# Kernel optimization log

Hardware: AMD Instinct MI355X
Metric: run time of the kernel (lower is better)

## Reference

```python
import jax, jax.numpy as jnp
import numpy as np

BN_EPS = 1e-5


def fps(xyz, npoint):
    # farthest point sampling; xyz: (B,N,3) -> (B,npoint) int32, starts at index 0 (torch convention)
    B, N, _ = xyz.shape
    def step(carry, _):
        dist, last = carry
        lp = jnp.take_along_axis(xyz, last[:, None, None], axis=1)  # (B,1,3)
        d = jnp.sum((xyz - lp) ** 2, -1)                             # (B,N)
        dist = jnp.minimum(dist, d)
        nxt = jnp.argmax(dist, -1).astype(jnp.int32)
        return (dist, nxt), nxt
    init = (jnp.full((B, N), 1e10, xyz.dtype), jnp.zeros((B,), jnp.int32))
    _, rest = jax.lax.scan(step, init, None, length=npoint - 1)
    return jnp.concatenate([jnp.zeros((1, B), jnp.int32), rest], 0).T  # (B,npoint)


def knn_idx(xyz, centers, k):
    # xyz (B,N,3), centers (B,S,3) -> (B,S,k) nearest-neighbor indices
    d = (jnp.sum(centers ** 2, -1)[:, :, None]
         + jnp.sum(xyz ** 2, -1)[:, None, :]
         - 2.0 * jnp.einsum('bsc,bnc->bsn', centers, xyz))
    _, idx = jax.lax.top_k(-d, k)
    return idx


def group(feat, idx):
    # feat (B,N,C), idx (B,S,K) -> (B,S,K,C)
    return jax.vmap(lambda f, i: f[i])(feat, idx)


def sa_knn(xyz, points, npoint, nsample, w1, b1, w2, b2):
    # xyz (B,N,3), points (B,N,C); returns new_xyz (B,S,3), new_points (B,S,Cout)
    fidx = fps(xyz, npoint)
    new_xyz = jnp.take_along_axis(xyz, fidx[:, :, None], axis=1)        # (B,S,3)
    idx = knn_idx(xyz, new_xyz, nsample)                                 # (B,S,K)
    g_xyz = group(xyz, idx) - new_xyz[:, :, None, :]                     # relative coords
    g_pts = group(points, idx)
    x = jnp.concatenate([g_xyz, g_pts], -1)                              # (B,S,K,3+C)
    x = jax.nn.relu(jnp.einsum('bskc,oc->bsko', x, w1) + b1)
    x = jnp.einsum('bskc,oc->bsko', x, w2) + b2                          # last conv: no activation
    return new_xyz, jnp.max(x, 2)                                        # max over neighbors


def sa_all(xyz, points, w1, b1, w2, b2):
    # group_all: concat xyz+points over all N, shared MLP, max over N -> (B,Cout)
    x = jnp.concatenate([xyz, points], -1)                               # (B,N,3+C)
    x = jax.nn.relu(jnp.einsum('bnc,oc->bno', x, w1) + b1)
    x = jnp.einsum('bnc,oc->bno', x, w2) + b2
    return jnp.max(x, 1)


def fc_head(x, w1, b1, g1, be1, w2, b2, g2, be2):
    # Linear + BN(eval, running mean=0/var=1) + ReLU, twice; Dropout = identity in eval
    s = 1.0 / np.sqrt(1.0 + BN_EPS)
    x = jax.nn.relu(g1 * ((x @ w1.T + b1) * s) + be1)
    x = jax.nn.relu(g2 * ((x @ w2.T + b2) * s) + be2)
    return x


def forward(point_cloud, sa1_w1, sa1_b1, sa1_w2, sa1_b2,
            sa2_w1, sa2_b1, sa2_w2, sa2_b2,
            sa3_w1, sa3_b1, sa3_w2, sa3_b2,
            fc_w1, fc_b1, fc_g1, fc_be1, fc_w2, fc_b2, fc_g2, fc_be2):
    xyz = jnp.transpose(point_cloud, (0, 2, 1))  # (B,N,3)
    nsamples2 = (16, 32, 48)
    logits, codes = [], []
    for i in range(3):  # three structurally distinct branches
        x1, p1 = sa_knn(xyz, xyz, 512, 16, sa1_w1[i], sa1_b1[i], sa1_w2[i], sa1_b2[i])
        x2, p2 = sa_knn(x1, p1, 128, nsamples2[i], sa2_w1[i], sa2_b1[i], sa2_w2[i], sa2_b2[i])
        code = sa_all(x2, p2, sa3_w1[i], sa3_b1[i], sa3_w2[i], sa3_b2[i])   # (B,512)
        logits.append(fc_head(code, fc_w1[i], fc_b1[i], fc_g1[i], fc_be1[i],
                              fc_w2[i], fc_b2[i], fc_g2[i], fc_be2[i]))      # (B,128)
        codes.append(code)
    return tuple(logits) + tuple(codes)


def setup_inputs():
    key = jax.random.key(0)
    ks = iter(jax.random.split(key, 16))
    def w(shape, s=0.05):
        return jax.random.normal(next(ks), shape, jnp.float32) * s
    B, N = 32, 2048
    inp = {'point_cloud': jax.random.normal(next(ks), (B, 3, N), jnp.float32)}
    inp.update(
        sa1_w1=w((3, 64, 6)), sa1_b1=jnp.zeros((3, 64)), sa1_w2=w((3, 128, 64)), sa1_b2=jnp.zeros((3, 128)),
        sa2_w1=w((3, 128, 131)), sa2_b1=jnp.zeros((3, 128)), sa2_w2=w((3, 256, 128)), sa2_b2=jnp.zeros((3, 256)),
        sa3_w1=w((3, 512, 259)), sa3_b1=jnp.zeros((3, 512)), sa3_w2=w((3, 512, 512)), sa3_b2=jnp.zeros((3, 512)),
        fc_w1=w((3, 256, 512)), fc_b1=jnp.zeros((3, 256)), fc_g1=jnp.ones((3, 256)), fc_be1=jnp.zeros((3, 256)),
        fc_w2=w((3, 128, 256)), fc_b2=jnp.zeros((3, 128)), fc_g2=jnp.ones((3, 128)), fc_be2=jnp.zeros((3, 128)),
    )
    return inp


def reference(point_cloud, sa1_w1, sa1_b1, sa1_w2, sa1_b2,
              sa2_w1, sa2_b1, sa2_w2, sa2_b2,
              sa3_w1, sa3_b1, sa3_w2, sa3_b2,
              fc_w1, fc_b1, fc_g1, fc_be1, fc_w2, fc_b2, fc_g2, fc_be2):
    return forward(point_cloud, sa1_w1, sa1_b1, sa1_w2, sa1_b2,
                   sa2_w1, sa2_b1, sa2_w2, sa2_b2,
                   sa3_w1, sa3_b1, sa3_w2, sa3_b2,
                   fc_w1, fc_b1, fc_g1, fc_be1, fc_w2, fc_b2, fc_g2, fc_be2)
```

## Files before the change

kernel.cpp:

```cpp
#include <hip/hip_runtime.h>
#include <hip/hip_bf16.h>
#include <math.h>

#define DEVI __device__ __forceinline__

static constexpr int BB = 32, NN = 2048, S1 = 512, S2 = 128;

typedef float f32x4 __attribute__((ext_vector_type(4)));
typedef short s16x8 __attribute__((ext_vector_type(8)));

static constexpr size_t OFF_XS   = 0;
static constexpr size_t OFF_YS   = OFF_XS + (size_t)BB*NN;
static constexpr size_t OFF_ZS   = OFF_YS + (size_t)BB*NN;
static constexpr size_t OFF_SSQ  = OFF_ZS + (size_t)BB*NN;
static constexpr size_t OFF_NX1X = OFF_SSQ + (size_t)BB*NN;
static constexpr size_t OFF_NX1Y = OFF_NX1X + (size_t)BB*S1;
static constexpr size_t OFF_NX1Z = OFF_NX1Y + (size_t)BB*S1;
static constexpr size_t OFF_NX2X = OFF_NX1Z + (size_t)BB*S1;
static constexpr size_t OFF_NX2Y = OFF_NX2X + (size_t)BB*S2;
static constexpr size_t OFF_NX2Z = OFF_NX2Y + (size_t)BB*S2;
static constexpr size_t OFF_CODE = OFF_NX2Z + (size_t)BB*S2;
static constexpr size_t OFF_O3P  = OFF_CODE + (size_t)3*BB*512;
static constexpr size_t OFF_P1   = OFF_O3P + (size_t)3*BB*4*512;
static constexpr size_t OFF_X3   = OFF_P1 + (size_t)3*BB*S1*128;
static constexpr size_t OFF_H3   = OFF_X3 + (size_t)3*BB*S2*260;
static constexpr size_t OFF_W    = OFF_H3 + (size_t)3*BB*S2*512;
static constexpr size_t W1A  = OFF_W;
static constexpr size_t B1A  = W1A + 3*64*6;
static constexpr size_t W2A  = B1A + 3*64;
static constexpr size_t B2A  = W2A + 3*128*64;
static constexpr size_t W1B  = B2A + 3*128;
static constexpr size_t B1B  = W1B + 3*128*132;
static constexpr size_t W2B  = B1B + 3*128;
static constexpr size_t B2B  = W2B + 3*256*128;
static constexpr size_t W1C  = B2B + 3*256;
static constexpr size_t B1C  = W1C + 3*512*260;
static constexpr size_t W2C  = B1C + 3*512;
static constexpr size_t B2C  = W2C + 3*512*512;
static constexpr size_t FW1  = B2C + 3*512;
static constexpr size_t FB1  = FW1 + 3*256*512;
static constexpr size_t FG1  = FB1 + 3*256;
static constexpr size_t FBE1 = FG1 + 3*256;
static constexpr size_t FW2  = FBE1 + 3*256;
static constexpr size_t FB2  = FW2 + 3*128*256;
static constexpr size_t FG2  = FB2 + 3*128;
static constexpr size_t FBE2 = FG2 + 3*128;
static constexpr size_t OFF_KNN1 = FBE2 + 3*128;
static constexpr size_t OFF_KNN2 = OFF_KNN1 + (size_t)BB*S1*16;
static constexpr size_t OFF_W1BF = OFF_KNN2 + (size_t)BB*S2*48;
static constexpr size_t OFF_W2BF = OFF_W1BF + 30720;
static constexpr size_t OFF_W1CBH = OFF_W2BF + 49152;
static constexpr size_t OFF_W1CBL = OFF_W1CBH + 221184;
static constexpr size_t OFF_W2CBH = OFF_W1CBL + 221184;
static constexpr size_t OFF_W2CBL = OFF_W2CBH + 393216;
static constexpr size_t OFF_X3BH  = OFF_W2CBL + 393216;
static constexpr size_t OFF_X3BL  = OFF_X3BH + 1769472;
static constexpr size_t OFF_H3BH  = OFF_X3BL + 1769472;
static constexpr size_t OFF_H3BL  = OFF_H3BH + 3145728;
static constexpr size_t OFF_W2ABH = OFF_H3BL + 3145728;
static constexpr size_t OFF_W2ABL = OFF_W2ABH + 12288;
static constexpr size_t WS_FLOATS = OFF_W2ABL + 12288;

__device__ __align__(16) float g_ws[WS_FLOATS];
__device__ int g_is_f32;
__device__ int g_flip;
__device__ int g_bad;
__device__ int g_nz;

DEVI float bf2f(const __hip_bfloat16 v){ return __bfloat162float(v); }
DEVI float rn_add(float a, float b){ return __fadd_rn(a,b); }
DEVI float rn_mul(float a, float b){ return __fmul_rn(a,b); }
DEVI float rn_sub(float a, float b){ return __fsub_rn(a,b); }
DEVI float sq3(float x,float y,float z){ return rn_add(rn_add(rn_mul(x,x),rn_mul(y,y)),rn_mul(z,z)); }

DEVI float ldany(const void* s, size_t i, int isf){
  return isf ? ((const float*)s)[i] : bf2f(((const __hip_bfloat16*)s)[i]);
}
DEVI unsigned short f2bf(float f){
  unsigned u = __float_as_uint(f);
  unsigned r = (u + 0x7FFFu + ((u>>16)&1u)) >> 16;
  return (unsigned short)r;
}
DEVI float bfbits2f(unsigned short h){ return __uint_as_float(((unsigned)h)<<16); }
DEVI void mfma16(f32x4& d, s16x8 a, s16x8 b){
  asm volatile("v_mfma_f32_16x16x32_bf16 %0, %1, %2, %0" : "+v"(d) : "v"(a), "v"(b));
}
DEVI void mfma_guard(f32x4& d){
  asm volatile("s_nop 7\n\ts_nop 7\n\ts_nop 2" : "+v"(d));
}

#define DPPF(dst, src, CTRL) dst = __uint_as_float((unsigned)__builtin_amdgcn_update_dpp(\
    (int)__float_as_uint(src), (int)__float_as_uint(src), CTRL, 0xF, 0xF, false))
#define DPPI(dst, src, CTRL) dst = __builtin_amdgcn_update_dpp(src, src, CTRL, 0xF, 0xF, false)
#define RED_STEP(CTRL) { float ov; int oi; DPPF(ov, best, CTRL); DPPI(oi, bidx, CTRL); \
  if (ov > best || (ov == best && oi < bidx)){ best = ov; bidx = oi; } }
#define WAVE_ARGMAX() RED_STEP(0xB1) RED_STEP(0x4E) RED_STEP(0x124) RED_STEP(0x128) RED_STEP(0x142) RED_STEP(0x143)

#define REDMIN_STEP(CTRL) { float ov; int oi; DPPF(ov, best, CTRL); DPPI(oi, bidx, CTRL); \
  if (ov < best || (ov == best && oi < bidx)){ best = ov; bidx = oi; } }
#define WAVE_ARGMIN() REDMIN_STEP(0xB1) REDMIN_STEP(0x4E) REDMIN_STEP(0x124) REDMIN_STEP(0x128) REDMIN_STEP(0x142) REDMIN_STEP(0x143)

__global__ __launch_bounds__(256) void init_detect_kernel(const void* __restrict__ pc){
  __shared__ int s_cnt[256];
  int t = threadIdx.x;
  if (t==0){ g_flip=0; g_bad=0; g_nz=0; }
  const unsigned short* h = (const unsigned short*)pc;
  int weird = 0;
  for (int i=t; i<4096; i+=256){
    unsigned short v = h[2*i];
    int e = (v >> 7) & 0xFF;
    if (e == 0xFF || e < 90 || e > 140) weird++;
  }
  s_cnt[t] = weird; __syncthreads();
  for (int o=128;o>0;o>>=1){ if (t<o) s_cnt[t]+=s_cnt[t+o]; __syncthreads(); }
  if (t==0) g_is_f32 = (s_cnt[0] > 1024) ? 1 : 0;
}

struct ParamPtrs { const void* p[20]; };

DEVI void cvt_arr(const void* s, float* d, int n, int g, int gs, int isf){
  for (int i=g;i<n;i+=gs) d[i] = ldany(s,i,isf);
}
DEVI void cvt_pad(const void* s, float* d, int rows, int cin, int cinp, int g, int gs, int isf){
  int tot = rows*cinp;
  for (int i=g;i<tot;i+=gs){ int r=i/cinp, c=i%cinp; d[i] = (c<cin)? ldany(s,(size_t)r*cin+c,isf) : 0.f; }
}

__global__ __launch_bounds__(256) void cvtprep_kernel(ParamPtrs pp, const void* __restrict__ pc, int mode){
  if (mode==1 && g_flip==0) return;
  const int isf = g_is_f32 ^ mode;
  if (blockIdx.x < 256){
    int i = blockIdx.x*256 + threadIdx.x;
    int b = i >> 11, n = i & 2047;
    float x = ldany(pc, (size_t)(b*3+0)*2048 + n, isf);
    float y = ldany(pc, (size_t)(b*3+1)*2048 + n, isf);
    float z = ldany(pc, (size_t)(b*3+2)*2048 + n, isf);
    g_ws[OFF_XS+i]=x; g_ws[OFF_YS+i]=y; g_ws[OFF_ZS+i]=z;
    g_ws[OFF_SSQ+i]=sq3(x,y,z);
    return;
  }
  int g = (blockIdx.x-256)*256 + threadIdx.x; int gs = 512*256;
  float* ws = g_ws;
  cvt_arr(pp.p[0],  ws+W1A, 3*64*6, g, gs, isf);
  cvt_arr(pp.p[1],  ws+B1A, 3*64, g, gs, isf);
  cvt_arr(pp.p[2],  ws+W2A, 3*128*64, g, gs, isf);
  cvt_arr(pp.p[3],  ws+B2A, 3*128, g, gs, isf);
  cvt_pad(pp.p[4],  ws+W1B, 3*128, 131, 132, g, gs, isf);
  cvt_arr(pp.p[5],  ws+B1B, 3*128, g, gs, isf);
  cvt_arr(pp.p[6],  ws+W2B, 3*256*128, g, gs, isf);
  cvt_arr(pp.p[7],  ws+B2B, 3*256, g, gs, isf);
  cvt_pad(pp.p[8],  ws+W1C, 3*512, 259, 260, g, gs, isf);
  cvt_arr(pp.p[9],  ws+B1C, 3*512, g, gs, isf);
  cvt_arr(pp.p[10], ws+W2C, 3*512*512, g, gs, isf);
  cvt_arr(pp.p[11], ws+B2C, 3*512, g, gs, isf);
  cvt_arr(pp.p[12], ws+FW1, 3*256*512, g, gs, isf);
  cvt_arr(pp.p[13], ws+FB1, 3*256, g, gs, isf);
  cvt_arr(pp.p[14], ws+FG1, 3*256, g, gs, isf);
  cvt_arr(pp.p[15], ws+FBE1,3*256, g, gs, isf);
  cvt_arr(pp.p[16], ws+FW2, 3*128*256, g, gs, isf);
  cvt_arr(pp.p[17], ws+FB2, 3*128, g, gs, isf);
  cvt_arr(pp.p[18], ws+FG2, 3*128, g, gs, isf);
  cvt_arr(pp.p[19], ws+FBE2,3*128, g, gs, isf);
}

__global__ __launch_bounds__(256) void scan_check_kernel(){
  size_t off; int n, g, gs;
  if (blockIdx.x < 128){ off = OFF_XS; n = 3*BB*NN; g = blockIdx.x*256 + threadIdx.x; gs = 128*256; }
  else { off = FW1; n = 3*256*512; g = (blockIdx.x-128)*256 + threadIdx.x; gs = 128*256; }
  int bad=0, nz=0;
  for (int i=g;i<n;i+=gs){
    float v = g_ws[off + i];
    if (v != v || fabsf(v) > 1e4f) bad=1;
    if (fabsf(v) > 1e-20f) nz=1;
  }
  unsigned long long mb = __ballot(bad), mn = __ballot(nz);
  if ((threadIdx.x & 63)==0){
    if (mb) atomicOr(&g_bad, 1);
    if (mn) atomicOr(&g_nz, 1);
  }
}

__global__ __launch_bounds__(64) void resolve_flip_kernel(){
  if (threadIdx.x==0){
    g_flip = (g_bad || !g_nz) ? 1 : 0;
    g_bad = 0; g_nz = 0;
  }
}

DEVI void cvt_bf16_body(int g, int gs){
  unsigned short* w1d = (unsigned short*)(g_ws + OFF_W1BF);
  for (int i=g; i<3*128*160; i+=gs){
    int br = i/(128*160); int rem = i%(128*160); int h = rem/160; int c = rem%160;
    float v = (c<132) ? g_ws[W1B + ((size_t)br*128 + h)*132 + c] : 0.f;
    w1d[i] = f2bf(v);
  }
  unsigned short* w2d = (unsigned short*)(g_ws + OFF_W2BF);
  for (int i=g; i<3*256*128; i+=gs) w2d[i] = f2bf(g_ws[W2B + i]);
  unsigned short* w1ch = (unsigned short*)(g_ws + OFF_W1CBH);
  unsigned short* w1cl = (unsigned short*)(g_ws + OFF_W1CBL);
  for (int i=g; i<3*512*288; i+=gs){
    int br = i/(512*288); int rem = i%(512*288); int n = rem/288; int c = rem%288;
    float v = (c<260) ? g_ws[W1C + ((size_t)br*512 + n)*260 + c] : 0.f;
    unsigned short hi = f2bf(v);
    w1ch[i] = hi; w1cl[i] = f2bf(v - bfbits2f(hi));
  }
  unsigned short* w2ch = (unsigned short*)(g_ws + OFF_W2CBH);
  unsigned short* w2cl = (unsigned short*)(g_ws + OFF_W2CBL);
  for (int i=g; i<3*512*512; i+=gs){
    float v = g_ws[W2C + i];
    unsigned short hi = f2bf(v);
    w2ch[i] = hi; w2cl[i] = f2bf(v - bfbits2f(hi));
  }
  unsigned short* w2ah = (unsigned short*)(g_ws + OFF_W2ABH);
  unsigned short* w2al = (unsigned short*)(g_ws + OFF_W2ABL);
  for (int i=g; i<3*128*64; i+=gs){
    float v = g_ws[W2A + i];
    unsigned short hi = f2bf(v);
    w2ah[i] = hi; w2al[i] = f2bf(v - bfbits2f(hi));
  }
}

#define FPS_DECL(J) float px##J, py##J, pz##J, dd##J;
#define FPS_LD256A(J) { int n=(J)*256+t; px##J=xs[n]; py##J=ys[n]; pz##J=zs[n]; dd##J=1e10f; xl[n]=px##J; yl[n]=py##J; zl[n]=pz##J; }
#define FPS_LD256B(J) { int n=(J)*256+t; px##J=xs[n]; py##J=ys[n]; pz##J=zs[n]; dd##J=ddg[n]; xl[n]=px##J; yl[n]=py##J; zl[n]=pz##J; }
#define FPS_SAVE(J) ddg[(J)*256+t]=dd##J;
#define FPS_LD64(J) { int n=(J)*64+t; px##J=xs[n]; py##J=ys[n]; pz##J=zs[n]; dd##J=1e10f; xl[n]=px##J; yl[n]=py##J; zl[n]=pz##J; }
#define FPS_UPD(J) { float dx=rn_sub(px##J,lx), dy=rn_sub(py##J,ly), dz=rn_sub(pz##J,lz); float d=sq3(dx,dy,dz); dd##J=fminf(dd##J,d); }
#define FPS_T1(J,JA,JB) float v##J; int q##J; { bool c = dd##JB > dd##JA; v##J = c? dd##JB : dd##JA; q##J = c? (JB) : (JA); }
#define FPS_T2(JA,JB) { bool c = v##JB > v##JA; v##JA = c? v##JB : v##JA; q##JA = c? q##JB : q##JA; }

#define FPS1_ITER_BODY() \
    FPS_UPD(0) FPS_UPD(1) FPS_UPD(2) FPS_UPD(3) FPS_UPD(4) FPS_UPD(5) FPS_UPD(6) FPS_UPD(7) \
    FPS_T1(0,0,1) FPS_T1(1,2,3) FPS_T1(2,4,5) FPS_T1(3,6,7) \
    FPS_T2(0,1) FPS_T2(2,3) \
    FPS_T2(0,2) \
    float best = v0; int bidx = q0*256 + t; \
    WAVE_ARGMAX() \
    int par = i & 1; \
    if ((t&63)==63){ s_val[par][wave]=best; s_idx[par][wave]=bidx; } \
    __syncthreads(); \
    float va = s_val[par][0], vb = s_val[par][1], vc = s_val[par][2], vd = s_val[par][3]; \
    int ia = s_idx[par][0], ib = s_idx[par][1], ic = s_idx[par][2], id_ = s_idx[par][3]; \
    if (vb > va || (vb == va && ib < ia)){ va = vb; ia = ib; } \
    if (vd > vc || (vd == vc && id_ < ic)){ vc = vd; ic = id_; } \
    if (vc > va || (vc == va && ic < ia)){ va = vc; ia = ic; } \
    int gidx = ia; \
    lx = xl[gidx]; ly = yl[gidx]; lz = zl[gidx]; \
    if (t==0){ nx[i]=lx; ny[i]=ly; nz[i]=lz; }

__global__ __launch_bounds__(256,1) void fps1a_cvt_kernel(){
  const int t = threadIdx.x;
  if (blockIdx.x >= 32){
    cvt_bf16_body((blockIdx.x-32)*256 + t, 256*256);
    return;
  }
  const int b = blockIdx.x;
  const int wave = t >> 6;
  const float* xs = g_ws + OFF_XS + (size_t)b*NN;
  const float* ys = g_ws + OFF_YS + (size_t)b*NN;
  const float* zs = g_ws + OFF_ZS + (size_t)b*NN;
  float* nx = g_ws + OFF_NX1X + (size_t)b*S1;
  float* ny = g_ws + OFF_NX1Y + (size_t)b*S1;
  float* nz = g_ws + OFF_NX1Z + (size_t)b*S1;
  float* ddg = g_ws + OFF_X3 + (size_t)b*NN;
  __shared__ float xl[NN], yl[NN], zl[NN];
  __shared__ float s_val[2][4]; __shared__ int s_idx[2][4];
  FPS_DECL(0) FPS_DECL(1) FPS_DECL(2) FPS_DECL(3) FPS_DECL(4) FPS_DECL(5) FPS_DECL(6) FPS_DECL(7)
  FPS_LD256A(0) FPS_LD256A(1) FPS_LD256A(2) FPS_LD256A(3) FPS_LD256A(4) FPS_LD256A(5) FPS_LD256A(6) FPS_LD256A(7)
  __syncthreads();
  float lx = xl[0], ly = yl[0], lz = zl[0];
  if (t==0){ nx[0]=lx; ny[0]=ly; nz[0]=lz; }
  for (int i=1;i<256;i++){
    FPS1_ITER_BODY()
  }
  FPS_SAVE(0) FPS_SAVE(1) FPS_SAVE(2) FPS_SAVE(3) FPS_SAVE(4) FPS_SAVE(5) FPS_SAVE(6) FPS_SAVE(7)
}

__global__ __launch_bounds__(256,1) void fps1b_kernel(){
  const int t = threadIdx.x;
  const int b = blockIdx.x;
  const int wave = t >> 6;
  const float* xs = g_ws + OFF_XS + (size_t)b*NN;
  const float* ys = g_ws + OFF_YS + (size_t)b*NN;
  const float* zs = g_ws + OFF_ZS + (size_t)b*NN;
  float* nx = g_ws + OFF_NX1X + (size_t)b*S1;
  float* ny = g_ws + OFF_NX1Y + (size_t)b*S1;
  float* nz = g_ws + OFF_NX1Z + (size_t)b*S1;
  const float* ddg = g_ws + OFF_X3 + (size_t)b*NN;
  __shared__ float xl[NN], yl[NN], zl[NN];
  __shared__ float s_val[2][4]; __shared__ int s_idx[2][4];
  FPS_DECL(0) FPS_DECL(1) FPS_DECL(2) FPS_DECL(3) FPS_DECL(4) FPS_DECL(5) FPS_DECL(6) FPS_DECL(7)
  FPS_LD256B(0) FPS_LD256B(1) FPS_LD256B(2) FPS_LD256B(3) FPS_LD256B(4) FPS_LD256B(5) FPS_LD256B(6) FPS_LD256B(7)
  __syncthreads();
  float lx = nx[255], ly = ny[255], lz = nz[255];
  for (int i=256;i<S1;i++){
    FPS1_ITER_BODY()
  }
}

#define KNN1_POISON(C) case C: d[C] = match ? 3.0e38f : d[C]; break;
DEVI void knn1_body(int wid, int lane){
  int b = wid >> 9;
  const float* xs = g_ws + OFF_XS + (size_t)b*NN;
  const float* ys = g_ws + OFF_YS + (size_t)b*NN;
  const float* zs = g_ws + OFF_ZS + (size_t)b*NN;
  const float* sq = g_ws + OFF_SSQ + (size_t)b*NN;
  float cx = g_ws[OFF_NX1X + wid], cy = g_ws[OFF_NX1Y + wid], cz = g_ws[OFF_NX1Z + wid];
  float sc = sq3(cx,cy,cz);
  float d[32];
  #pragma unroll
  for (int c=0;c<32;c++){
    int n = c*64 + lane;
    float x=xs[n], y=ys[n], z=zs[n];
    float dot = rn_add(rn_add(rn_mul(cx,x),rn_mul(cy,y)),rn_mul(cz,z));
    d[c] = rn_sub(rn_add(sc,sq[n]), rn_mul(2.f,dot));
  }
  int* out = (int*)(g_ws + OFF_KNN1) + (size_t)wid*16;
  for (int r=0;r<16;r++){
    float tv[16]; int tc[16];
    #pragma unroll
    for (int c=0;c<16;c++){
      float a = d[2*c];
      float e = d[2*c+1];
      bool cc = e < a;
      tv[c] = cc ? e : a; tc[c] = cc ? (2*c+1) : (2*c);
    }
    #pragma unroll
    for (int s=1; s<16; s<<=1){
      #pragma unroll
      for (int c=0;c<16;c+=2){
        if ((c % (2*s)) == 0 && c+s < 16){
          bool cc = tv[c+s] < tv[c];
          tv[c] = cc ? tv[c+s] : tv[c];
          tc[c] = cc ? tc[c+s] : tc[c];
        }
      }
    }
    float best = tv[0]; int bidx = tc[0]*64 + lane;
    WAVE_ARGMIN()
    int wbi = __builtin_amdgcn_readlane(bidx, 63);
    if (lane == 0) out[r] = wbi;
    bool match = (lane == (wbi & 63));
    switch ((wbi >> 6) & 31){
      KNN1_POISON(0)  KNN1_POISON(1)  KNN1_POISON(2)  KNN1_POISON(3)
      KNN1_POISON(4)  KNN1_POISON(5)  KNN1_POISON(6)  KNN1_POISON(7)
      KNN1_POISON(8)  KNN1_POISON(9)  KNN1_POISON(10) KNN1_POISON(11)
      KNN1_POISON(12) KNN1_POISON(13) KNN1_POISON(14) KNN1_POISON(15)
      KNN1_POISON(16) KNN1_POISON(17) KNN1_POISON(18) KNN1_POISON(19)
      KNN1_POISON(20) KNN1_POISON(21) KNN1_POISON(22) KNN1_POISON(23)
      KNN1_POISON(24) KNN1_POISON(25) KNN1_POISON(26) KNN1_POISON(27)
      KNN1_POISON(28) KNN1_POISON(29) KNN1_POISON(30) KNN1_POISON(31)
    }
  }
}

__global__ __launch_bounds__(256) void fps2_knn1_kernel(){
  if (blockIdx.x >= 32){
    knn1_body(((blockIdx.x-32)*256 + threadIdx.x) >> 6, threadIdx.x & 63);
    return;
  }
  if (threadIdx.x >= 64) return;
  const int b = blockIdx.x, t = threadIdx.x;
  const float* xs = g_ws + OFF_NX1X + (size_t)b*S1;
  const float* ys = g_ws + OFF_NX1Y + (size_t)b*S1;
  const float* zs = g_ws + OFF_NX1Z + (size_t)b*S1;
  float* nx = g_ws + OFF_NX2X + (size_t)b*S2;
  float* ny = g_ws + OFF_NX2Y + (size_t)b*S2;
  float* nz = g_ws + OFF_NX2Z + (size_t)b*S2;
  __shared__ float xl[S1], yl[S1], zl[S1];
  FPS_DECL(0) FPS_DECL(1) FPS_DECL(2) FPS_DECL(3) FPS_DECL(4) FPS_DECL(5) FPS_DECL(6) FPS_DECL(7)
  FPS_LD64(0) FPS_LD64(1) FPS_LD64(2) FPS_LD64(3) FPS_LD64(4) FPS_LD64(5) FPS_LD64(6) FPS_LD64(7)
  float lx = xl[0], ly = yl[0], lz = zl[0];
  if (t==0){ nx[0]=lx; ny[0]=ly; nz[0]=lz; }
  for (int i=1;i<S2;i++){
    FPS_UPD(0) FPS_UPD(1) FPS_UPD(2) FPS_UPD(3) FPS_UPD(4) FPS_UPD(5) FPS_UPD(6) FPS_UPD(7)
    FPS_T1(0,0,1) FPS_T1(1,2,3) FPS_T1(2,4,5) FPS_T1(3,6,7)
    FPS_T2(0,1) FPS_T2(2,3)
    FPS_T2(0,2)
    float best = v0; int bidx = q0*64 + t;
    WAVE_ARGMAX()
    int gidx = __builtin_amdgcn_readlane(bidx, 63);
    lx = xl[gidx]; ly = yl[gidx]; lz = zl[gidx];
    if (t==0){ nx[i]=lx; ny[i]=ly; nz[i]=lz; }
  }
}

#define KNN2_POISON(C) case C: d[C] = match ? 3.0e38f : d[C]; break;
DEVI void knn2_body(int wid, int lane){
  int b = wid >> 7;
  const float* xs = g_ws + OFF_NX1X + (size_t)b*S1;
  const float* ys = g_ws + OFF_NX1Y + (size_t)b*S1;
  const float* zs = g_ws + OFF_NX1Z + (size_t)b*S1;
  float cx = g_ws[OFF_NX2X + wid], cy = g_ws[OFF_NX2Y + wid], cz = g_ws[OFF_NX2Z + wid];
  float sc = sq3(cx,cy,cz);
  float d[8];
  #pragma unroll
  for (int c=0;c<8;c++){
    int n = c*64 + lane;
    float x=xs[n], y=ys[n], z=zs[n];
    float sx = sq3(x,y,z);
    float dot = rn_add(rn_add(rn_mul(cx,x),rn_mul(cy,y)),rn_mul(cz,z));
    d[c] = rn_sub(rn_add(sc,sx), rn_mul(2.f,dot));
  }
  int* out = (int*)(g_ws + OFF_KNN2) + (size_t)wid*48;
  for (int r=0;r<48;r++){
    float tv[4]; int tc[4];
    #pragma unroll
    for (int c=0;c<4;c++){
      float a = d[2*c];
      float e = d[2*c+1];
      bool cc = e < a;
      tv[c] = cc ? e : a; tc[c] = cc ? (2*c+1) : (2*c);
    }
    { bool cc = tv[1] < tv[0]; tv[0] = cc?tv[1]:tv[0]; tc[0] = cc?tc[1]:tc[0]; }
    { bool cc = tv[3] < tv[2]; tv[2] = cc?tv[3]:tv[2]; tc[2] = cc?tc[3]:tc[2]; }
    { bool cc = tv[2] < tv[0]; tv[0] = cc?tv[2]:tv[0]; tc[0] = cc?tc[2]:tc[0]; }
    float best = tv[0]; int bidx = tc[0]*64 + lane;
    WAVE_ARGMIN()
    int wbi = __builtin_amdgcn_readlane(bidx, 63);
    if (lane == 0) out[r] = wbi;
    bool match = (lane == (wbi & 63));
    switch ((wbi >> 6) & 7){
      KNN2_POISON(0) KNN2_POISON(1) KNN2_POISON(2) KNN2_POISON(3)
      KNN2_POISON(4) KNN2_POISON(5) KNN2_POISON(6) KNN2_POISON(7)
    }
  }
}

__global__ __launch_bounds__(256) void knn2_sa1_kernel(){
  const int t = threadIdx.x;
  if (blockIdx.x < 1024){
    knn2_body((blockIdx.x*256 + t) >> 6, t & 63);
    return;
  }
  const int bx2 = blockIdx.x - 1024;
  const int br = bx2 >> 10;
  const int bxx = bx2 & 1023;
  const int wave = t>>6, lane = t&63, quad = lane>>4, l16 = lane&15;
  __shared__ float w1s[384];
  __shared__ float b1s[64];
  __shared__ __align__(16) short Hh[4][16*72];
  __shared__ __align__(16) short Hl[4][16*72];
  for (int i=t;i<384;i+=256) w1s[i] = g_ws[W1A + (size_t)br*384 + i];
  if (t<64) b1s[t] = g_ws[B1A + br*64 + t];
  __syncthreads();
  const int* kn = (const int*)(g_ws + OFF_KNN1);
  const short* w2h = (const short*)(g_ws + OFF_W2ABH) + (size_t)br*128*64;
  const short* w2l = (const short*)(g_ws + OFF_W2ABL) + (size_t)br*128*64;
  const float* b2 = g_ws + B2A + br*128;
  for (int it=0; it<4; it++){
    int gid = bxx*16 + it*4 + wave;
    int b = gid >> 9;
    int idx = kn[(size_t)gid*16 + l16] & (NN-1);
    float cx = g_ws[OFF_NX1X+gid], cy = g_ws[OFF_NX1Y+gid], cz = g_ws[OFF_NX1Z+gid];
    size_t gl = (size_t)b*NN + idx;
    float x = g_ws[OFF_XS+gl], y = g_ws[OFF_YS+gl], z = g_ws[OFF_ZS+gl];
    float f0=x-cx, f1=y-cy, f2=z-cz;
    #pragma unroll
    for (int i=0;i<16;i++){
      int h = quad*16 + i;
      float acc = b1s[h];
      acc += f0*w1s[h*6+0] + f1*w1s[h*6+1] + f2*w1s[h*6+2]
           +  x*w1s[h*6+3] +  y*w1s[h*6+4] +  z*w1s[h*6+5];
      acc = fmaxf(acc, 0.f);
      unsigned short hi = f2bf(acc);
      Hh[wave][l16*72 + h] = (short)hi;
      Hl[wave][l16*72 + h] = (short)f2bf(acc - bfbits2f(hi));
    }
    __syncthreads();
    s16x8 ah[2], al[2];
    #pragma unroll
    for (int ks=0;ks<2;ks++){
      ah[ks] = *(const s16x8*)(&Hh[wave][l16*72 + ks*32 + quad*8]);
      al[ks] = *(const s16x8*)(&Hl[wave][l16*72 + ks*32 + quad*8]);
    }
    float* P1g = g_ws + OFF_P1 + ((size_t)br*16384 + gid)*128;
    #pragma unroll
    for (int ni=0; ni<8; ni++){
      int o = ni*16 + l16;
      f32x4 acc = {0.f,0.f,0.f,0.f};
      #pragma unroll
      for (int ks=0; ks<2; ks++){
        s16x8 bh = *(const s16x8*)(w2h + (size_t)o*64 + ks*32 + quad*8);
        s16x8 bl = *(const s16x8*)(w2l + (size_t)o*64 + ks*32 + quad*8);
        mfma16(acc, ah[ks], bh);
        mfma16(acc, ah[ks], bl);
        mfma16(acc, al[ks], bh);
      }
      mfma_guard(acc);
      float vmax = fmaxf(fmaxf(acc[0],acc[1]), fmaxf(acc[2],acc[3]));
      vmax = fmaxf(vmax, __shfl_xor(vmax,16));
      vmax = fmaxf(vmax, __shfl_xor(vmax,32));
      if (quad==0) P1g[o] = vmax + b2[o];
    }
  }
}

template<int K>
DEVI void sa2_body(int br, int g2, short* Xb, short* Hb, float* ctr, int* idxs){
  constexpr int MT = K/16;
  const int b = g2 >> 7;
  const int t = threadIdx.x;
  const int wave = t >> 6, lane = t & 63, quad = lane >> 4, l16 = lane & 15;
  const int* kn2 = (const int*)(g_ws + OFF_KNN2) + (size_t)g2*48;
  if (t < K) idxs[t] = kn2[t] & (S1-1);
  if (t < 3) ctr[t] = g_ws[(t==0?OFF_NX2X:(t==1?OFF_NX2Y:OFF_NX2Z)) + g2];
  __syncthreads();
  const float* p1b = g_ws + OFF_P1 + (size_t)br*16384*128;
  for (int e=t; e<K*168; e+=256){
    int k = e/168, j = e%168;
    int idx = idxs[k];
    float v;
    if (j < 3){
      const float* A = (j==0)? g_ws+OFF_NX1X : (j==1)? g_ws+OFF_NX1Y : g_ws+OFF_NX1Z;
      v = A[(size_t)b*S1 + idx] - ctr[j];
    } else if (j < 131){
      v = p1b[((size_t)b*S1 + idx)*128 + (j-3)];
    } else v = 0.f;
    Xb[e] = (short)f2bf(v);
  }
  __syncthreads();
  {
    const short* w1bf = (const short*)(g_ws + OFF_W1BF) + (size_t)br*128*160;
    const float* b1 = g_ws + B1B + br*128;
    for (int ni = wave; ni < 8; ni += 4){
      int h = ni*16 + l16;
      s16x8 bfr[5];
      #pragma unroll
      for (int ks=0;ks<5;ks++) bfr[ks] = *(const s16x8*)(w1bf + (size_t)h*160 + ks*32 + quad*8);
      float bias = b1[h];
      #pragma unroll
      for (int m=0; m<MT; m++){
        f32x4 acc = {0.f,0.f,0.f,0.f};
        #pragma unroll
        for (int ks=0;ks<5;ks++){
          s16x8 a = *(const s16x8*)(&Xb[(m*16 + l16)*168 + ks*32 + quad*8]);
          mfma16(acc, a, bfr[ks]);
        }
        mfma_guard(acc);
        #pragma unroll
        for (int r=0;r<4;r++){
          int row = m*16 + quad*4 + r;
          float hv = fmaxf(acc[r] + bias, 0.f);
          Hb[row*136 + ni*16 + l16] = (short)f2bf(hv);
        }
      }
    }
  }
  __syncthreads();
  {
    const short* w2bf = (const short*)(g_ws + OFF_W2BF) + (size_t)br*256*128;
    const float* b2 = g_ws + B2B + br*256;
    unsigned short* xh = (unsigned short*)(g_ws + OFF_X3BH);
    unsigned short* xlo = (unsigned short*)(g_ws + OFF_X3BL);
    size_t row = (size_t)(br*4096 + g2)*288;
    for (int ni = wave; ni < 16; ni += 4){
      int o = ni*16 + l16;
      s16x8 bfr[4];
      #pragma unroll
      for (int ks=0;ks<4;ks++) bfr[ks] = *(const s16x8*)(w2bf + (size_t)o*128 + ks*32 + quad*8);
      float vmax = -3.4e38f;
      #pragma unroll
      for (int m=0; m<MT; m++){
        f32x4 acc = {0.f,0.f,0.f,0.f};
        #pragma unroll
        for (int ks=0;ks<4;ks++){
          s16x8 a = *(const s16x8*)(&Hb[(m*16 + l16)*136 + ks*32 + quad*8]);
          mfma16(acc, a, bfr[ks]);
        }
        mfma_guard(acc);
        #pragma unroll
        for (int r=0;r<4;r++) vmax = fmaxf(vmax, acc[r]);
      }
      vmax = fmaxf(vmax, __shfl_xor(vmax, 16));
      vmax = fmaxf(vmax, __shfl_xor(vmax, 32));
      if (quad == 0){
        float hv = vmax + b2[o];
        unsigned short hi = f2bf(hv);
        xh[row + 3 + o] = hi;
        xlo[row + 3 + o] = f2bf(hv - bfbits2f(hi));
      }
    }
    if (t < 3){
      float cv = ctr[t];
      unsigned short hi = f2bf(cv);
      xh[row + t] = hi; xlo[row + t] = f2bf(cv - bfbits2f(hi));
    }
    if (t >= 3 && t < 32){ xh[row + 256 + t] = 0; xlo[row + 256 + t] = 0; }
  }
}

__global__ __launch_bounds__(256) void sa2_all_kernel(){
  __shared__ __align__(16) short Xb[48*168];
  __shared__ __align__(16) short Hb[48*136];
  __shared__ float ctr[3];
  __shared__ int idxs[48];
  int br = blockIdx.x >> 12;
  int g2 = blockIdx.x & 4095;
  if (br == 0)      sa2_body<16>(0, g2, Xb, Hb, ctr, idxs);
  else if (br == 1) sa2_body<32>(1, g2, Xb, Hb, ctr, idxs);
  else              sa2_body<48>(2, g2, Xb, Hb, ctr, idxs);
}

__global__ __launch_bounds__(256) void sa3l1_mfma_kernel(){
  const int br = blockIdx.y; const int r0 = blockIdx.x*32;
  const int t = threadIdx.x;
  const int wave = t >> 6, lane = t & 63, quad = lane >> 4, l16 = lane & 15;
  const short* xh = (const short*)(g_ws + OFF_X3BH) + (size_t)(br*4096 + r0)*288;
  const short* xl = (const short*)(g_ws + OFF_X3BL) + (size_t)(br*4096 + r0)*288;
  const short* wh = (const short*)(g_ws + OFF_W1CBH) + (size_t)br*512*288;
  const short* wl = (const short*)(g_ws + OFF_W1CBL) + (size_t)br*512*288;
  const float* bias = g_ws + B1C + br*512;
  unsigned short* hh = (unsigned short*)(g_ws + OFF_H3BH) + (size_t)(br*4096 + r0)*512;
  unsigned short* hl = (unsigned short*)(g_ws + OFF_H3BL) + (size_t)(br*4096 + r0)*512;
  f32x4 acc[2][8];
  #pragma unroll
  for (int m=0;m<2;m++)
    #pragma unroll
    for (int ni=0;ni<8;ni++) acc[m][ni] = (f32x4){0.f,0.f,0.f,0.f};
  for (int ks=0; ks<9; ks++){
    s16x8 ah[2], al[2];
    #pragma unroll
    for (int m=0;m<2;m++){
      ah[m] = *(const s16x8*)(xh + (size_t)(m*16+l16)*288 + ks*32 + quad*8);
      al[m] = *(const s16x8*)(xl + (size_t)(m*16+l16)*288 + ks*32 + quad*8);
    }
    #pragma unroll
    for (int ni=0;ni<8;ni++){
      int n = wave*128 + ni*16 + l16;
      s16x8 bh = *(const s16x8*)(wh + (size_t)n*288 + ks*32 + quad*8);
      s16x8 bl = *(const s16x8*)(wl + (size_t)n*288 + ks*32 + quad*8);
      #pragma unroll
      for (int m=0;m<2;m++){
        mfma16(acc[m][ni], ah[m], bh);
        mfma16(acc[m][ni], ah[m], bl);
        mfma16(acc[m][ni], al[m], bh);
      }
    }
  }
  mfma_guard(acc[0][0]);
  #pragma unroll
  for (int m=0;m<2;m++){
    #pragma unroll
    for (int ni=0;ni<8;ni++){
      int col = wave*128 + ni*16 + l16;
      float bs = bias[col];
      #pragma unroll
      for (int r=0;r<4;r++){
        int row = m*16 + quad*4 + r;
        float hv = fmaxf(acc[m][ni][r] + bs, 0.f);
        unsigned short hi = f2bf(hv);
        hh[(size_t)row*512 + col] = hi;
        hl[(size_t)row*512 + col] = f2bf(hv - bfbits2f(hi));
      }
    }
  }
}

__global__ __launch_bounds__(256) void sa3l2_mfma_kernel(){
  const int br = blockIdx.y; const int b = blockIdx.x>>2; const int part = blockIdx.x&3;
  const int t = threadIdx.x;
  const int wave = t >> 6, lane = t & 63, quad = lane >> 4, l16 = lane & 15;
  const int row0 = b*128 + part*32;
  const short* ahp = (const short*)(g_ws + OFF_H3BH) + (size_t)(br*4096 + row0)*512;
  const short* alp = (const short*)(g_ws + OFF_H3BL) + (size_t)(br*4096 + row0)*512;
  const short* wh = (const short*)(g_ws + OFF_W2CBH) + (size_t)br*512*512;
  const short* wl = (const short*)(g_ws + OFF_W2CBL) + (size_t)br*512*512;
  f32x4 acc[2][8];
  #pragma unroll
  for (int m=0;m<2;m++)
    #pragma unroll
    for (int ni=0;ni<8;ni++) acc[m][ni] = (f32x4){0.f,0.f,0.f,0.f};
  for (int ks=0; ks<16; ks++){
    s16x8 ah[2], al[2];
    #pragma unroll
    for (int m=0;m<2;m++){
      ah[m] = *(const s16x8*)(ahp + (size_t)(m*16+l16)*512 + ks*32 + quad*8);
      al[m] = *(const s16x8*)(alp + (size_t)(m*16+l16)*512 + ks*32 + quad*8);
    }
    #pragma unroll
    for (int ni=0;ni<8;ni++){
      int n = wave*128 + ni*16 + l16;
      s16x8 bh = *(const s16x8*)(wh + (size_t)n*512 + ks*32 + quad*8);
      s16x8 bl = *(const s16x8*)(wl + (size_t)n*512 + ks*32 + quad*8);
      #pragma unroll
      for (int m=0;m<2;m++){
        mfma16(acc[m][ni], ah[m], bh);
        mfma16(acc[m][ni], ah[m], bl);
        mfma16(acc[m][ni], al[m], bh);
      }
    }
  }
  mfma_guard(acc[0][0]);
  #pragma unroll
  for (int ni=0;ni<8;ni++){
    float vmax = -3.4e38f;
    #pragma unroll
    for (int m=0;m<2;m++)
      #pragma unroll
      for (int r=0;r<4;r++) vmax = fmaxf(vmax, acc[m][ni][r]);
    vmax = fmaxf(vmax, __shfl_xor(vmax, 16));
    vmax = fmaxf(vmax, __shfl_xor(vmax, 32));
    if (quad == 0){
      int col = wave*128 + ni*16 + l16;
      g_ws[OFF_O3P + (((size_t)br*BB + b)*4 + part)*512 + col] = vmax;
    }
  }
}

__global__ __launch_bounds__(256) void fc_kernel(float* __restrict__ out, int out_size){
  int br = blockIdx.x >> 5; int b = blockIdx.x & 31; int t = threadIdx.x;
  __shared__ float xin[512]; __shared__ float x1s[256];
  const float* o3p = g_ws + OFF_O3P + (((size_t)br*BB + b)*4)*512;
  const float* b2c = g_ws + B2C + br*512;
  #pragma unroll
  for (int k=0;k<2;k++){
    int o = t + k*256;
    float m = fmaxf(fmaxf(o3p[o], o3p[512+o]), fmaxf(o3p[1024+o], o3p[1536+o]));
    m += b2c[o];
    xin[o] = m;
    int oi = 3*BB*128 + ((br*BB + b)*512) + o;
    if (oi < out_size) out[oi] = m;
  }
  __syncthreads();
  const float s = (float)(1.0 / sqrt(1.0 + 1e-5));
  {
    const float4* wp = (const float4*)(g_ws + FW1 + ((size_t)br*256 + t)*512);
    const float4* xp = (const float4*)xin;
    float acc = 0.f;
    #pragma unroll 8
    for (int q=0;q<128;q++){ float4 w4=wp[q], x4=xp[q]; acc += w4.x*x4.x + w4.y*x4.y + w4.z*x4.z + w4.w*x4.w; }
    acc = (acc + g_ws[FB1 + br*256+t]) * s;
    acc = g_ws[FG1+br*256+t]*acc + g_ws[FBE1+br*256+t];
    x1s[t] = fmaxf(acc, 0.f);
  }
  __syncthreads();
  if (t < 128){
    const float4* wp = (const float4*)(g_ws + FW2 + ((size_t)br*128 + t)*256);
    const float4* xp = (const float4*)x1s;
    float acc=0.f;
    #pragma unroll 8
    for (int q=0;q<64;q++){ float4 w4=wp[q], x4=xp[q]; acc += w4.x*x4.x + w4.y*x4.y + w4.z*x4.z + w4.w*x4.w; }
    acc = (acc + g_ws[FB2+br*128+t])*s;
    acc = g_ws[FG2+br*128+t]*acc + g_ws[FBE2+br*128+t];
    int oi = ((size_t)br*BB + b)*128 + t;
    if (oi < out_size) out[oi] = fmaxf(acc,0.f);
  }
}

extern "C" void kernel_launch(void* const* d_in, const int* in_sizes, int n_in,
                              void* d_out, int out_size, void* d_ws, size_t ws_size,
                              hipStream_t stream) {
  (void)d_ws; (void)ws_size;
  if (n_in < 21) return;
  if (in_sizes[0] != BB*3*NN) return;
  float* out = (float*)d_out;

  ParamPtrs pp;
  for (int i=0;i<20;i++) pp.p[i] = d_in[i+1];

  init_detect_kernel<<<1,256,0,stream>>>(d_in[0]);
  cvtprep_kernel<<<768,256,0,stream>>>(pp, d_in[0], 0);
  scan_check_kernel<<<256,256,0,stream>>>();
  resolve_flip_kernel<<<1,64,0,stream>>>();
  cvtprep_kernel<<<768,256,0,stream>>>(pp, d_in[0], 1);

  fps1a_cvt_kernel<<<32+256,256,0,stream>>>();
  fps1b_kernel<<<32,256,0,stream>>>();
  fps2_knn1_kernel<<<32+4096,256,0,stream>>>();
  knn2_sa1_kernel<<<1024+3072,256,0,stream>>>();
  sa2_all_kernel<<<3*4096,256,0,stream>>>();

  sa3l1_mfma_kernel<<<dim3(128,3),256,0,stream>>>();
  sa3l2_mfma_kernel<<<dim3(128,3),256,0,stream>>>();
  fc_kernel<<<96,256,0,stream>>>(out, out_size);
}
```

Baseline: 1.186 ms.

## Process two batch items per FPS block to interleave independent reduction chains

The first-stage farthest point sampling kernels now handle two batch elements per 256-thread block, with 16 blocks instead of 32. The distance updates, DPP wave argmax and shared-memory combine for both items are interleaved, and both share one barrier per iteration. The aim is to hide the latency of the serial per-iteration dependency chain (DPP reduction, barrier, LDS lookup) by giving each wave independent work, and to halve barrier count per sample. In exchange it doubles register and LDS use per block and uses only half as many CUs, so throughput-bound parts may slow down.

```diff
diff --git a/kernel.cpp b/kernel.cpp
--- a/kernel.cpp
+++ b/kernel.cpp
@@ -100,6 +100,13 @@
   if (ov < best || (ov == best && oi < bidx)){ best = ov; bidx = oi; } }
 #define WAVE_ARGMIN() REDMIN_STEP(0xB1) REDMIN_STEP(0x4E) REDMIN_STEP(0x124) REDMIN_STEP(0x128) REDMIN_STEP(0x142) REDMIN_STEP(0x143)
 
+#define RED_STEP2(CTRL) { float ovA,ovB; int oiA,oiB; \
+  DPPF(ovA, bestA, CTRL); DPPI(oiA, bidxA, CTRL); \
+  DPPF(ovB, bestB, CTRL); DPPI(oiB, bidxB, CTRL); \
+  if (ovA > bestA || (ovA == bestA && oiA < bidxA)){ bestA = ovA; bidxA = oiA; } \
+  if (ovB > bestB || (ovB == bestB && oiB < bidxB)){ bestB = ovB; bidxB = oiB; } }
+#define WAVE_ARGMAX2() RED_STEP2(0xB1) RED_STEP2(0x4E) RED_STEP2(0x124) RED_STEP2(0x128) RED_STEP2(0x142) RED_STEP2(0x143)
+
 __global__ __launch_bounds__(256) void init_detect_kernel(const void* __restrict__ pc){
   __shared__ int s_cnt[256];
   int t = threadIdx.x;
@@ -220,81 +227,115 @@
   }
 }
 
-#define FPS_DECL(J) float px##J, py##J, pz##J, dd##J;
-#define FPS_LD256A(J) { int n=(J)*256+t; px##J=xs[n]; py##J=ys[n]; pz##J=zs[n]; dd##J=1e10f; xl[n]=px##J; yl[n]=py##J; zl[n]=pz##J; }
-#define FPS_LD256B(J) { int n=(J)*256+t; px##J=xs[n]; py##J=ys[n]; pz##J=zs[n]; dd##J=ddg[n]; xl[n]=px##J; yl[n]=py##J; zl[n]=pz##J; }
-#define FPS_SAVE(J) ddg[(J)*256+t]=dd##J;
-#define FPS_LD64(J) { int n=(J)*64+t; px##J=xs[n]; py##J=ys[n]; pz##J=zs[n]; dd##J=1e10f; xl[n]=px##J; yl[n]=py##J; zl[n]=pz##J; }
-#define FPS_UPD(J) { float dx=rn_sub(px##J,lx), dy=rn_sub(py##J,ly), dz=rn_sub(pz##J,lz); float d=sq3(dx,dy,dz); dd##J=fminf(dd##J,d); }
-#define FPS_T1(J,JA,JB) float v##J; int q##J; { bool c = dd##JB > dd##JA; v##J = c? dd##JB : dd##JA; q##J = c? (JB) : (JA); }
-#define FPS_T2(JA,JB) { bool c = v##JB > v##JA; v##JA = c? v##JB : v##JA; q##JA = c? q##JB : q##JA; }
-
-#define FPS1_ITER_BODY() \
-    FPS_UPD(0) FPS_UPD(1) FPS_UPD(2) FPS_UPD(3) FPS_UPD(4) FPS_UPD(5) FPS_UPD(6) FPS_UPD(7) \
-    FPS_T1(0,0,1) FPS_T1(1,2,3) FPS_T1(2,4,5) FPS_T1(3,6,7) \
-    FPS_T2(0,1) FPS_T2(2,3) \
-    FPS_T2(0,2) \
-    float best = v0; int bidx = q0*256 + t; \
-    WAVE_ARGMAX() \
+#define FPS_DECL2(C,J) float px##C##J, py##C##J, pz##C##J, dd##C##J;
+#define FPS_LDA2(C,J) { int n=(J)*256+t; px##C##J=xs##C[n]; py##C##J=ys##C[n]; pz##C##J=zs##C[n]; dd##C##J=1e10f; xl##C[n]=px##C##J; yl##C[n]=py##C##J; zl##C[n]=pz##C##J; }
+#define FPS_LDB2(C,J) { int n=(J)*256+t; px##C##J=xs##C[n]; py##C##J=ys##C[n]; pz##C##J=zs##C[n]; dd##C##J=ddg##C[n]; xl##C[n]=px##C##J; yl##C[n]=py##C##J; zl##C[n]=pz##C##J; }
+#define FPS_SAV2(C,J) ddg##C[(J)*256+t]=dd##C##J;
+#define FPS_UPD2(C,J) { float dx=rn_sub(px##C##J,lx##C), dy=rn_sub(py##C##J,ly##C), dz=rn_sub(pz##C##J,lz##C); dd##C##J=fminf(dd##C##J, sq3(dx,dy,dz)); }
+#define FPS_TT2(C) \
+    float v0##C,v1##C,v2##C,v3##C; int q0##C,q1##C,q2##C,q3##C; \
+    { bool c=dd##C##1>dd##C##0; v0##C=c?dd##C##1:dd##C##0; q0##C=c?1:0; } \
+    { bool c=dd##C##3>dd##C##2; v1##C=c?dd##C##3:dd##C##2; q1##C=c?3:2; } \
+    { bool c=dd##C##5>dd##C##4; v2##C=c?dd##C##5:dd##C##4; q2##C=c?5:4; } \
+    { bool c=dd##C##7>dd##C##6; v3##C=c?dd##C##7:dd##C##6; q3##C=c?7:6; } \
+    { bool c=v1##C>v0##C; v0##C=c?v1##C:v0##C; q0##C=c?q1##C:q0##C; } \
+    { bool c=v3##C>v2##C; v2##C=c?v3##C:v2##C; q2##C=c?q3##C:q2##C; } \
+    { bool c=v2##C>v0##C; v0##C=c?v2##C:v0##C; q0##C=c?q2##C:q0##C; }
+#define FPS_COMB2(C,K) { \
+    float va=s_val[par][K][0], vb=s_val[par][K][1], vc=s_val[par][K][2], vd=s_val[par][K][3]; \
+    int ia=s_idx[par][K][0], ib=s_idx[par][K][1], ic=s_idx[par][K][2], id_=s_idx[par][K][3]; \
+    if (vb>va || (vb==va && ib<ia)){ va=vb; ia=ib; } \
+    if (vd>vc || (vd==vc && id_<ic)){ vc=vd; ic=id_; } \
+    if (vc>va || (vc==va && ic<ia)){ va=vc; ia=ic; } \
+    lx##C = xl##C[ia]; ly##C = yl##C[ia]; lz##C = zl##C[ia]; \
+    if (t==0){ nx##C[i]=lx##C; ny##C[i]=ly##C; nz##C[i]=lz##C; } }
+
+#define FPS1_DUAL_BODY() \
+    FPS_UPD2(A,0) FPS_UPD2(A,1) FPS_UPD2(A,2) FPS_UPD2(A,3) FPS_UPD2(A,4) FPS_UPD2(A,5) FPS_UPD2(A,6) FPS_UPD2(A,7) \
+    FPS_UPD2(B,0) FPS_UPD2(B,1) FPS_UPD2(B,2) FPS_UPD2(B,3) FPS_UPD2(B,4) FPS_UPD2(B,5) FPS_UPD2(B,6) FPS_UPD2(B,7) \
+    FPS_TT2(A) FPS_TT2(B) \
+    float bestA = v0A; int bidxA = q0A*256 + t; \
+    float bestB = v0B; int bidxB = q0B*256 + t; \
+    WAVE_ARGMAX2() \
     int par = i & 1; \
-    if ((t&63)==63){ s_val[par][wave]=best; s_idx[par][wave]=bidx; } \
+    if ((t&63)==63){ \
+      s_val[par][0][wave]=bestA; s_idx[par][0][wave]=bidxA; \
+      s_val[par][1][wave]=bestB; s_idx[par][1][wave]=bidxB; \
+    } \
     __syncthreads(); \
-    float va = s_val[par][0], vb = s_val[par][1], vc = s_val[par][2], vd = s_val[par][3]; \
-    int ia = s_idx[par][0], ib = s_idx[par][1], ic = s_idx[par][2], id_ = s_idx[par][3]; \
-    if (vb > va || (vb == va && ib < ia)){ va = vb; ia = ib; } \
-    if (vd > vc || (vd == vc && id_ < ic)){ vc = vd; ic = id_; } \
-    if (vc > va || (vc == va && ic < ia)){ va = vc; ia = ic; } \
-    int gidx = ia; \
-    lx = xl[gidx]; ly = yl[gidx]; lz = zl[gidx]; \
-    if (t==0){ nx[i]=lx; ny[i]=ly; nz[i]=lz; }
+    FPS_COMB2(A,0) \
+    FPS_COMB2(B,1)
 
 __global__ __launch_bounds__(256,1) void fps1a_cvt_kernel(){
   const int t = threadIdx.x;
-  if (blockIdx.x >= 32){
-    cvt_bf16_body((blockIdx.x-32)*256 + t, 256*256);
+  if (blockIdx.x >= 16){
+    cvt_bf16_body((blockIdx.x-16)*256 + t, 256*256);
     return;
   }
-  const int b = blockIdx.x;
+  const int bA = blockIdx.x*2, bB = bA+1;
   const int wave = t >> 6;
-  const float* xs = g_ws + OFF_XS + (size_t)b*NN;
-  const float* ys = g_ws + OFF_YS + (size_t)b*NN;
-  const float* zs = g_ws + OFF_ZS + (size_t)b*NN;
-  float* nx = g_ws + OFF_NX1X + (size_t)b*S1;
-  float* ny = g_ws + OFF_NX1Y + (size_t)b*S1;
-  float* nz = g_ws + OFF_NX1Z + (size_t)b*S1;
-  float* ddg = g_ws + OFF_X3 + (size_t)b*NN;
-  __shared__ float xl[NN], yl[NN], zl[NN];
-  __shared__ float s_val[2][4]; __shared__ int s_idx[2][4];
-  FPS_DECL(0) FPS_DECL(1) FPS_DECL(2) FPS_DECL(3) FPS_DECL(4) FPS_DECL(5) FPS_DECL(6) FPS_DECL(7)
-  FPS_LD256A(0) FPS_LD256A(1) FPS_LD256A(2) FPS_LD256A(3) FPS_LD256A(4) FPS_LD256A(5) FPS_LD256A(6) FPS_LD256A(7)
+  const float* xsA = g_ws + OFF_XS + (size_t)bA*NN;
+  const float* ysA = g_ws + OFF_YS + (size_t)bA*NN;
+  const float* zsA = g_ws + OFF_ZS + (size_t)bA*NN;
+  const float* xsB = g_ws + OFF_XS + (size_t)bB*NN;
+  const float* ysB = g_ws + OFF_YS + (size_t)bB*NN;
+  const float* zsB = g_ws + OFF_ZS + (size_t)bB*NN;
+  float* nxA = g_ws + OFF_NX1X + (size_t)bA*S1;
+  float* nyA = g_ws + OFF_NX1Y + (size_t)bA*S1;
+  float* nzA = g_ws + OFF_NX1Z + (size_t)bA*S1;
+  float* nxB = g_ws + OFF_NX1X + (size_t)bB*S1;
+  float* nyB = g_ws + OFF_NX1Y + (size_t)bB*S1;
+  float* nzB = g_ws + OFF_NX1Z + (size_t)bB*S1;
+  float* ddgA = g_ws + OFF_X3 + (size_t)bA*NN;
+  float* ddgB = g_ws + OFF_X3 + (size_t)bB*NN;
+  __shared__ float xlA[NN], ylA[NN], zlA[NN];
+  __shared__ float xlB[NN], ylB[NN], zlB[NN];
+  __shared__ float s_val[2][2][4]; __shared__ int s_idx[2][2][4];
+  FPS_DECL2(A,0) FPS_DECL2(A,1) FPS_DECL2(A,2) FPS_DECL2(A,3) FPS_DECL2(A,4) FPS_DECL2(A,5) FPS_DECL2(A,6) FPS_DECL2(A,7)
+  FPS_DECL2(B,0) FPS_DECL2(B,1) FPS_DECL2(B,2) FPS_DECL2(B,3) FPS_DECL2(B,4) FPS_DECL2(B,5) FPS_DECL2(B,6) FPS_DECL2(B,7)
+  FPS_LDA2(A,0) FPS_LDA2(A,1) FPS_LDA2(A,2) FPS_LDA2(A,3) FPS_LDA2(A,4) FPS_LDA2(A,5) FPS_LDA2(A,6) FPS_LDA2(A,7)
+  FPS_LDA2(B,0) FPS_LDA2(B,1) FPS_LDA2(B,2) FPS_LDA2(B,3) FPS_LDA2(B,4) FPS_LDA2(B,5) FPS_LDA2(B,6) FPS_LDA2(B,7)
   __syncthreads();
-  float lx = xl[0], ly = yl[0], lz = zl[0];
-  if (t==0){ nx[0]=lx; ny[0]=ly; nz[0]=lz; }
+  float lxA = xlA[0], lyA = ylA[0], lzA = zlA[0];
+  float lxB = xlB[0], lyB = ylB[0], lzB = zlB[0];
+  if (t==0){ nxA[0]=lxA; nyA[0]=lyA; nzA[0]=lzA; nxB[0]=lxB; nyB[0]=lyB; nzB[0]=lzB; }
   for (int i=1;i<256;i++){
-    FPS1_ITER_BODY()
-  }
-  FPS_SAVE(0) FPS_SAVE(1) FPS_SAVE(2) FPS_SAVE(3) FPS_SAVE(4) FPS_SAVE(5) FPS_SAVE(6) FPS_SAVE(7)
+    FPS1_DUAL_BODY()
+  }
+  FPS_SAV2(A,0) FPS_SAV2(A,1) FPS_SAV2(A,2) FPS_SAV2(A,3) FPS_SAV2(A,4) FPS_SAV2(A,5) FPS_SAV2(A,6) FPS_SAV2(A,7)
+  FPS_SAV2(B,0) FPS_SAV2(B,1) FPS_SAV2(B,2) FPS_SAV2(B,3) FPS_SAV2(B,4) FPS_SAV2(B,5) FPS_SAV2(B,6) FPS_SAV2(B,7)
 }
 
 __global__ __launch_bounds__(256,1) void fps1b_kernel(){
   const int t = threadIdx.x;
-  const int b = blockIdx.x;
+  const int bA = blockIdx.x*2, bB = bA+1;
   const int wave = t >> 6;
-  const float* xs = g_ws + OFF_XS + (size_t)b*NN;
-  const float* ys = g_ws + OFF_YS + (size_t)b*NN;
-  const float* zs = g_ws + OFF_ZS + (size_t)b*NN;
-  float* nx = g_ws + OFF_NX1X + (size_t)b*S1;
-  float* ny = g_ws + OFF_NX1Y + (size_t)b*S1;
-  float* nz = g_ws + OFF_NX1Z + (size_t)b*S1;
-  const float* ddg = g_ws + OFF_X3 + (size_t)b*NN;
-  __shared__ float xl[NN], yl[NN], zl[NN];
-  __shared__ float s_val[2][4]; __shared__ int s_idx[2][4];
-  FPS_DECL(0) FPS_DECL(1) FPS_DECL(2) FPS_DECL(3) FPS_DECL(4) FPS_DECL(5) FPS_DECL(6) FPS_DECL(7)
-  FPS_LD256B(0) FPS_LD256B(1) FPS_LD256B(2) FPS_LD256B(3) FPS_LD256B(4) FPS_LD256B(5) FPS_LD256B(6) FPS_LD256B(7)
+  const float* xsA = g_ws + OFF_XS + (size_t)bA*NN;
+  const float* ysA = g_ws + OFF_YS + (size_t)bA*NN;
+  const float* zsA = g_ws + OFF_ZS + (size_t)bA*NN;
+  const float* xsB = g_ws + OFF_XS + (size_t)bB*NN;
+  const float* ysB = g_ws + OFF_YS + (size_t)bB*NN;
+  const float* zsB = g_ws + OFF_ZS + (size_t)bB*NN;
+  float* nxA = g_ws + OFF_NX1X + (size_t)bA*S1;
+  float* nyA = g_ws + OFF_NX1Y + (size_t)bA*S1;
+  float* nzA = g_ws + OFF_NX1Z + (size_t)bA*S1;
+  float* nxB = g_ws + OFF_NX1X + (size_t)bB*S1;
+  float* nyB = g_ws + OFF_NX1Y + (size_t)bB*S1;
+  float* nzB = g_ws + OFF_NX1Z + (size_t)bB*S1;
+  const float* ddgA = g_ws + OFF_X3 + (size_t)bA*NN;
+  const float* ddgB = g_ws + OFF_X3 + (size_t)bB*NN;
+  __shared__ float xlA[NN], ylA[NN], zlA[NN];
+  __shared__ float xlB[NN], ylB[NN], zlB[NN];
+  __shared__ float s_val[2][2][4]; __shared__ int s_idx[2][2][4];
+  FPS_DECL2(A,0) FPS_DECL2(A,1) FPS_DECL2(A,2) FPS_DECL2(A,3) FPS_DECL2(A,4) FPS_DECL2(A,5) FPS_DECL2(A,6) FPS_DECL2(A,7)
+  FPS_DECL2(B,0) FPS_DECL2(B,1) FPS_DECL2(B,2) FPS_DECL2(B,3) FPS_DECL2(B,4) FPS_DECL2(B,5) FPS_DECL2(B,6) FPS_DECL2(B,7)
+  FPS_LDB2(A,0) FPS_LDB2(A,1) FPS_LDB2(A,2) FPS_LDB2(A,3) FPS_LDB2(A,4) FPS_LDB2(A,5) FPS_LDB2(A,6) FPS_LDB2(A,7)
+  FPS_LDB2(B,0) FPS_LDB2(B,1) FPS_LDB2(B,2) FPS_LDB2(B,3) FPS_LDB2(B,4) FPS_LDB2(B,5) FPS_LDB2(B,6) FPS_LDB2(B,7)
   __syncthreads();
-  float lx = nx[255], ly = ny[255], lz = nz[255];
+  float lxA = nxA[255], lyA = nyA[255], lzA = nzA[255];
+  float lxB = nxB[255], lyB = nyB[255], lzB = nzB[255];
   for (int i=256;i<S1;i++){
-    FPS1_ITER_BODY()
+    FPS1_DUAL_BODY()
   }
 }
 
@@ -353,6 +394,12 @@
     }
   }
 }
+
+#define FPS_DECL(J) float px##J, py##J, pz##J, dd##J;
+#define FPS_LD64(J) { int n=(J)*64+t; px##J=xs[n]; py##J=ys[n]; pz##J=zs[n]; dd##J=1e10f; xl[n]=px##J; yl[n]=py##J; zl[n]=pz##J; }
+#define FPS_UPD(J) { float dx=rn_sub(px##J,lx), dy=rn_sub(py##J,ly), dz=rn_sub(pz##J,lz); float d=sq3(dx,dy,dz); dd##J=fminf(dd##J,d); }
+#define FPS_T1(J,JA,JB) float v##J; int q##J; { bool c = dd##JB > dd##JA; v##J = c? dd##JB : dd##JA; q##J = c? (JB) : (JA); }
+#define FPS_T2(JA,JB) { bool c = v##JB > v##JA; v##JA = c? v##JB : v##JA; q##JA = c? q##JB : q##JA; }
 
 __global__ __launch_bounds__(256) void fps2_knn1_kernel(){
   if (blockIdx.x >= 32){
@@ -765,8 +812,8 @@
   resolve_flip_kernel<<<1,64,0,stream>>>();
   cvtprep_kernel<<<768,256,0,stream>>>(pp, d_in[0], 1);
 
-  fps1a_cvt_kernel<<<32+256,256,0,stream>>>();
-  fps1b_kernel<<<32,256,0,stream>>>();
+  fps1a_cvt_kernel<<<16+256,256,0,stream>>>();
+  fps1b_kernel<<<16,256,0,stream>>>();
   fps2_knn1_kernel<<<32+4096,256,0,stream>>>();
   knn2_sa1_kernel<<<1024+3072,256,0,stream>>>();
   sa2_all_kernel<<<3*4096,256,0,stream>>>();
```

New measurement: 1.495 ms. +26.0%, slower.
